# Optimization experiments

Measured on AMD Instinct MI355X. Metric: run time of the kernel, lower is better.

## Reference

```python
import jax, jax.numpy as jnp
import numpy as np

HIDDEN = 1024
N_HEAD = 16
D_HEAD = HIDDEN // N_HEAD


def setup_inputs() -> dict:
    key = jax.random.key(0)
    ks = jax.random.split(key, 12)
    B, S, H = 2, 2048, HIDDEN
    scale = 1.0 / np.sqrt(H)
    inp = {
        "q": jax.random.normal(ks[0], (B, S, H), jnp.float32),
        "k": jax.random.normal(ks[1], (B, S, H), jnp.float32),
        "v": jax.random.normal(ks[2], (B, S, H), jnp.float32),
        "mask": jnp.ones((B, 1, S, S), jnp.int32),
        "w_q": jax.random.normal(ks[3], (H, H), jnp.float32) * scale,
        "b_q": jnp.zeros((H,), jnp.float32),
        "w_k": jax.random.normal(ks[4], (H, H), jnp.float32) * scale,
        "b_k": jnp.zeros((H,), jnp.float32),
        "w_v": jax.random.normal(ks[5], (H, H), jnp.float32) * scale,
        "b_v": jnp.zeros((H,), jnp.float32),
        "w_o": jax.random.normal(ks[6], (H, H), jnp.float32) * scale,
        "b_o": jnp.zeros((H,), jnp.float32),
    }
    return inp


def reference(q, k, v, mask, w_q, b_q, w_k, b_k, w_v, b_v, w_o, b_o):
    B, Sq, H = q.shape
    Sk = k.shape[1]
    # projections (weights stored as [in, out])
    qh = (q @ w_q + b_q).reshape(B, Sq, N_HEAD, D_HEAD).transpose(0, 2, 1, 3)
    kh = (k @ w_k + b_k).reshape(B, Sk, N_HEAD, D_HEAD).transpose(0, 2, 1, 3)
    vh = (v @ w_v + b_v).reshape(B, Sk, N_HEAD, D_HEAD).transpose(0, 2, 1, 3)
    scores = jnp.einsum("bhqd,bhkd->bhqk", qh, kh) * (D_HEAD ** -0.5)
    scores = jnp.where(mask == 0, jnp.float32(-10000.0), scores)
    attn = jax.nn.softmax(scores, axis=-1)
    out = jnp.einsum("bhqk,bhkd->bhqd", attn, vh)
    out = out.transpose(0, 2, 1, 3).reshape(B, Sq, H)
    return out @ w_o + b_o
```

## Files before the change

kernel.cpp:

```cpp
#include <hip/hip_runtime.h>
#include <hip/hip_bf16.h>
#include <stdint.h>

#define S_LEN 2048
#define HID   1024
#define NHEAD 16
#define DHEAD 64
#define BATCH 2

#define QSCALE 0.18033688f
#define MASKNEG -14427.0f

typedef __bf16 bf16_t;
typedef __bf16 bf16x4 __attribute__((ext_vector_type(4)));
typedef __bf16 bf16x8 __attribute__((ext_vector_type(8)));
typedef float  f32x4  __attribute__((ext_vector_type(4)));


__device__ __forceinline__ void gl_lds16(const bf16_t* g, bf16_t* l) {
  __builtin_amdgcn_global_load_lds((const __attribute__((address_space(1))) void*)g,
                                   (__attribute__((address_space(3))) void*)l,
                                   16, 0, 0);
}

template<int TR, int TC>
__device__ __forceinline__ void stage_tile(const bf16_t* __restrict__ g, int ldg,
                                           bf16_t* lds, int wave, int lane) {
  constexpr int CH = TC / 8;
  constexpr int NINST = (TR * CH) / 64;
  #pragma unroll
  for (int i = wave; i < NINST; i += 4) {
    int slot = i * 64 + lane;
    int r  = slot / CH;
    int cs = slot & (CH - 1);
    int c  = cs ^ (r & (CH - 1));
    gl_lds16(g + (size_t)r * ldg + c * 8, lds + i * 512);
  }
}

template<int CH>
__device__ __forceinline__ bf16x8 frag_ld(const bf16_t* lds, int row, int kchunk) {
  int cs = kchunk ^ (row & (CH - 1));
  return *(const bf16x8*)(lds + (row * CH + cs) * 8);
}

__global__ __launch_bounds__(256) void cvt3(const float* __restrict__ q,
                                            const float* __restrict__ k,
                                            const float* __restrict__ v,
                                            bf16_t* __restrict__ qb,
                                            bf16_t* __restrict__ kb,
                                            bf16_t* __restrict__ vb) {
  int which = blockIdx.y;
  const float* src = which == 0 ? q : which == 1 ? k : v;
  bf16_t* dst = which == 0 ? qb : which == 1 ? kb : vb;
  size_t i = ((size_t)blockIdx.x * 256 + threadIdx.x) * 4;
  float4 u = *(const float4*)(src + i);
  bf16x4 o = {(bf16_t)u.x, (bf16_t)u.y, (bf16_t)u.z, (bf16_t)u.w};
  *(bf16x4*)(dst + i) = o;
}

__global__ __launch_bounds__(256) void transpose_w4(
    const float* __restrict__ w0, const float* __restrict__ w1,
    const float* __restrict__ w2, const float* __restrict__ w3,
    bf16_t* __restrict__ wt, int* __restrict__ flags) {
  if (blockIdx.x == 0 && blockIdx.y == 0 && blockIdx.z == 0) {
    flags[threadIdx.x] = -1;
    flags[threadIdx.x + 256] = -1;
  }
  __shared__ float t[64][65];
  const float* W = blockIdx.z == 0 ? w0 : blockIdx.z == 1 ? w1 : blockIdx.z == 2 ? w2 : w3;
  bf16_t* WT = wt + (size_t)blockIdx.z * HID * HID;
  int tx = threadIdx.x & 63, ty = threadIdx.x >> 6;
  int r0 = blockIdx.y * 64, c0 = blockIdx.x * 64;
  #pragma unroll
  for (int i = ty; i < 64; i += 4) t[i][tx] = W[(size_t)(r0 + i) * HID + c0 + tx];
  __syncthreads();
  #pragma unroll
  for (int i = ty; i < 64; i += 4) WT[(size_t)(c0 + i) * HID + r0 + tx] = (bf16_t)t[tx][i];
}

__global__ __launch_bounds__(256) void mask_flags(const int* __restrict__ mask,
                                                  int* __restrict__ flags) {
  int qtile = blockIdx.x, rg = blockIdx.y, b = blockIdx.z;
  const int* base = mask + (size_t)b * S_LEN * S_LEN
                  + (size_t)(qtile * 128 + rg * 16) * S_LEN;
  int tid = threadIdx.x;
  int kt = tid >> 4;
  int ok = 1;
  #pragma unroll
  for (int r = 0; r < 16; ++r) {
    const int4* p = (const int4*)(base + (size_t)r * S_LEN + tid * 8);
    int4 a = p[0], c = p[1];
    ok &= (a.x != 0) & (a.y != 0) & (a.z != 0) & (a.w != 0) &
          (c.x != 0) & (c.y != 0) & (c.z != 0) & (c.w != 0);
  }
  __shared__ int oks[16];
  if (tid < 16) oks[tid] = -1;
  __syncthreads();
  if (!ok) atomicAnd(&oks[kt], 0);
  __syncthreads();
  if (tid < 16 && oks[tid] == 0) atomicAnd(&flags[(b * 16 + qtile) * 16 + tid], 0);
}

__global__ __launch_bounds__(256) void qkv_gemm(
    const bf16_t* __restrict__ qb, const bf16_t* __restrict__ kb, const bf16_t* __restrict__ vb,
    const bf16_t* __restrict__ wT,
    const float* __restrict__ bq, const float* __restrict__ bk, const float* __restrict__ bv,
    bf16_t* __restrict__ Qh, bf16_t* __restrict__ Kh, bf16_t* __restrict__ VhT) {
  int mode = blockIdx.z;
  const bf16_t* A    = mode == 0 ? qb : mode == 1 ? kb : vb;
  const bf16_t* Bt   = wT + (size_t)mode * HID * HID;
  const float*  bias = mode == 0 ? bq : mode == 1 ? bk : bv;

  __shared__ __align__(16) bf16_t As[128 * 64];
  __shared__ __align__(16) bf16_t Bs[128 * 64];

  int tid = threadIdx.x, wave = tid >> 6, lane = tid & 63;
  int lane15 = lane & 15, quad = lane >> 4;
  int m0 = blockIdx.x * 128, n0 = blockIdx.y * 128;
  int wm = (wave >> 1) * 64, wn = (wave & 1) * 64;

  f32x4 zero4 = {0.f, 0.f, 0.f, 0.f};
  f32x4 acc[4][4];
  #pragma unroll
  for (int t = 0; t < 4; ++t)
    #pragma unroll
    for (int n = 0; n < 4; ++n) acc[t][n] = zero4;

  for (int k0 = 0; k0 < HID; k0 += 64) {
    stage_tile<128, 64>(A  + (size_t)m0 * HID + k0, HID, As, wave, lane);
    stage_tile<128, 64>(Bt + (size_t)n0 * HID + k0, HID, Bs, wave, lane);
    __syncthreads();
    #pragma unroll
    for (int kc = 0; kc < 2; ++kc) {
      bf16x8 af[4], bfr[4];
      #pragma unroll
      for (int t = 0; t < 4; ++t) af[t]  = frag_ld<8>(As, wm + t * 16 + lane15, kc * 4 + quad);
      #pragma unroll
      for (int n = 0; n < 4; ++n) bfr[n] = frag_ld<8>(Bs, wn + n * 16 + lane15, kc * 4 + quad);
      if (mode < 2) {
        #pragma unroll
        for (int t = 0; t < 4; ++t)
          #pragma unroll
          for (int n = 0; n < 4; ++n)
            acc[t][n] = __builtin_amdgcn_mfma_f32_16x16x32_bf16(af[t], bfr[n], acc[t][n], 0, 0, 0);
      } else {
        #pragma unroll
        for (int t = 0; t < 4; ++t)
          #pragma unroll
          for (int n = 0; n < 4; ++n)
            acc[t][n] = __builtin_amdgcn_mfma_f32_16x16x32_bf16(bfr[n], af[t], acc[t][n], 0, 0, 0);
      }
    }
    __syncthreads();
  }

  if (mode < 2) {
    float sc = (mode == 0) ? QSCALE : 1.0f;
    bf16_t* dst = (mode == 0 ? Qh : Kh);
    #pragma unroll
    for (int t = 0; t < 4; ++t) {
      #pragma unroll
      for (int n = 0; n < 4; ++n) {
        int col = n0 + wn + n * 16 + lane15;
        float bb = bias[col];
        #pragma unroll
        for (int i = 0; i < 4; ++i) {
          int row = m0 + wm + t * 16 + quad * 4 + i;
          bf16_t o = (bf16_t)((acc[t][n][i] + bb) * sc);
          int b = row >> 11, s = row & 2047;
          int h = col >> 6,  d = col & 63;
          dst[((size_t)(b * NHEAD + h) * S_LEN + s) * DHEAD + d] = o;
        }
      }
    }
  } else {
    #pragma unroll
    for (int n = 0; n < 4; ++n) {
      int dbase = n0 + wn + n * 16 + quad * 4;
      float4 bb4 = *(const float4*)(bias + dbase);
      #pragma unroll
      for (int t = 0; t < 4; ++t) {
        int token = m0 + wm + t * 16 + lane15;
        int b = token >> 11, s = token & 2047;
        #pragma unroll
        for (int i = 0; i < 4; ++i) {
          int dg = dbase + i;
          int h = dg >> 6, d = dg & 63;
          float bb = i == 0 ? bb4.x : i == 1 ? bb4.y : i == 2 ? bb4.z : bb4.w;
          VhT[((size_t)(b * NHEAD + h) * DHEAD + d) * S_LEN + s] = (bf16_t)(acc[t][n][i] + bb);
        }
      }
    }
  }
}

__global__ __launch_bounds__(256) void attn_kernel(
    const bf16_t* __restrict__ Qh, const bf16_t* __restrict__ Kh, const bf16_t* __restrict__ VhT,
    const int* __restrict__ mask, const int* __restrict__ flags,
    bf16_t* __restrict__ O) {
  __shared__ __align__(16) bf16_t Ks[2][64 * 64];
  __shared__ __align__(16) bf16_t VTs[2][80 * 64];
  __shared__ __align__(16) bf16_t Ps[128 * 64];

  int tid = threadIdx.x, wave = tid >> 6, lane = tid & 63;
  int lane15 = lane & 15, quad = lane >> 4;
  int bh = blockIdx.y, b = bh >> 4, h = bh & 15;
  int qt = blockIdx.x;
  int wrow = wave * 32;

  const bf16_t* Kbase = Kh + (size_t)bh * S_LEN * DHEAD;
  const bf16_t* Vbase = VhT + (size_t)bh * DHEAD * S_LEN;
  const int* flagrow = flags + (b * 16 + qt) * 16;

  if (tid < 64) {
    VTs[0][64 * 64 + tid] = (bf16_t)1.0f;
    VTs[1][64 * 64 + tid] = (bf16_t)1.0f;
  }

  stage_tile<128, 64>(Qh + ((size_t)bh * S_LEN + qt * 128) * DHEAD, DHEAD, Ps, wave, lane);
  stage_tile<64, 64>(Kbase, DHEAD, Ks[0], wave, lane);
  stage_tile<64, 64>(Vbase, S_LEN, VTs[0], wave, lane);
  __syncthreads();

  bf16x8 qa[2][2];
  #pragma unroll
  for (int kc = 0; kc < 2; ++kc)
    #pragma unroll
    for (int nq = 0; nq < 2; ++nq)
      qa[kc][nq] = frag_ld<8>(Ps, wrow + nq * 16 + lane15, kc * 4 + quad);

  f32x4 zero4 = {0.f, 0.f, 0.f, 0.f};
  f32x4 o_acc[2][5];
  #pragma unroll
  for (int nq = 0; nq < 2; ++nq)
    #pragma unroll
    for (int mt = 0; mt < 5; ++mt) o_acc[nq][mt] = zero4;

  int cur = 0;
  for (int kt = 0; kt < S_LEN / 64; ++kt) {
    if (kt + 1 < S_LEN / 64) {
      stage_tile<64, 64>(Kbase + (size_t)(kt + 1) * 64 * DHEAD, DHEAD, Ks[cur ^ 1], wave, lane);
      stage_tile<64, 64>(Vbase + (kt + 1) * 64, S_LEN, VTs[cur ^ 1], wave, lane);
    }
    const bf16_t* Kc = Ks[cur];
    const bf16_t* Vc = VTs[cur];

    f32x4 sa[2][4];
    {
      bf16x8 kf[4];
      #pragma unroll
      for (int mc = 0; mc < 4; ++mc) kf[mc] = frag_ld<8>(Kc, mc * 16 + lane15, quad);
      __builtin_amdgcn_s_setprio(1);
      #pragma unroll
      for (int nq = 0; nq < 2; ++nq)
        #pragma unroll
        for (int mc = 0; mc < 4; ++mc)
          sa[nq][mc] = __builtin_amdgcn_mfma_f32_16x16x32_bf16(kf[mc], qa[0][nq], zero4, 0, 0, 0);
      __builtin_amdgcn_s_setprio(0);
      #pragma unroll
      for (int mc = 0; mc < 4; ++mc) kf[mc] = frag_ld<8>(Kc, mc * 16 + lane15, 4 + quad);
      __builtin_amdgcn_s_setprio(1);
      #pragma unroll
      for (int nq = 0; nq < 2; ++nq)
        #pragma unroll
        for (int mc = 0; mc < 4; ++mc)
          sa[nq][mc] = __builtin_amdgcn_mfma_f32_16x16x32_bf16(kf[mc], qa[1][nq], sa[nq][mc], 0, 0, 0);
      __builtin_amdgcn_s_setprio(0);
    }

    if (flagrow[kt >> 1] == 0) {
      #pragma unroll
      for (int nq = 0; nq < 2; ++nq)
        #pragma unroll
        for (int mc = 0; mc < 4; ++mc)
          #pragma unroll
          for (int i = 0; i < 4; ++i) {
            int q = qt * 128 + wrow + nq * 16 + lane15;
            int c = kt * 64 + mc * 16 + quad * 4 + i;
            if (mask[(size_t)b * S_LEN * S_LEN + (size_t)q * S_LEN + c] == 0)
              sa[nq][mc][i] = MASKNEG;
          }
    }

    #pragma unroll
    for (int nq = 0; nq < 2; ++nq) {
      int q = wrow + nq * 16 + lane15;
      #pragma unroll
      for (int mc = 0; mc < 4; ++mc) {
        bf16x4 pk = {(bf16_t)exp2f(sa[nq][mc][0]), (bf16_t)exp2f(sa[nq][mc][1]),
                     (bf16_t)exp2f(sa[nq][mc][2]), (bf16_t)exp2f(sa[nq][mc][3])};
        int chunk = mc * 2 + (quad >> 1);
        int slot = chunk ^ (q & 7);
        *(bf16x4*)(Ps + q * 64 + slot * 8 + (quad & 1) * 4) = pk;
      }
    }

    #pragma unroll
    for (int kc = 0; kc < 2; ++kc) {
      bf16x8 vf[5], pf[2];
      #pragma unroll
      for (int mt = 0; mt < 5; ++mt) vf[mt] = frag_ld<8>(Vc, mt * 16 + lane15, kc * 4 + quad);
      #pragma unroll
      for (int nq = 0; nq < 2; ++nq) pf[nq] = frag_ld<8>(Ps, wrow + nq * 16 + lane15, kc * 4 + quad);
      __builtin_amdgcn_s_setprio(1);
      #pragma unroll
      for (int nq = 0; nq < 2; ++nq)
        #pragma unroll
        for (int mt = 0; mt < 5; ++mt)
          o_acc[nq][mt] = __builtin_amdgcn_mfma_f32_16x16x32_bf16(vf[mt], pf[nq], o_acc[nq][mt], 0, 0, 0);
      __builtin_amdgcn_s_setprio(0);
    }

    __syncthreads();
    cur ^= 1;
  }

  #pragma unroll
  for (int nq = 0; nq < 2; ++nq) {
    float lval = __shfl(o_acc[nq][4][0], lane15);
    float inv = 1.0f / lval;
    int s = qt * 128 + wrow + nq * 16 + lane15;
    size_t orow = ((size_t)b * S_LEN + s) * HID + h * DHEAD;
    #pragma unroll
    for (int mt = 0; mt < 4; ++mt) {
      bf16x4 ov = {(bf16_t)(o_acc[nq][mt][0] * inv), (bf16_t)(o_acc[nq][mt][1] * inv),
                   (bf16_t)(o_acc[nq][mt][2] * inv), (bf16_t)(o_acc[nq][mt][3] * inv)};
      *(bf16x4*)(O + orow + mt * 16 + quad * 4) = ov;
    }
  }
}

__global__ __launch_bounds__(256) void oproj_gemm(
    const bf16_t* __restrict__ A, const bf16_t* __restrict__ Bt,
    const float* __restrict__ bias, float* __restrict__ out) {
  __shared__ __align__(16) bf16_t As[128 * 64];
  __shared__ __align__(16) bf16_t Bs[128 * 64];

  int tid = threadIdx.x, wave = tid >> 6, lane = tid & 63;
  int lane15 = lane & 15, quad = lane >> 4;
  int m0 = blockIdx.x * 128, n0 = blockIdx.y * 128;
  int wm = (wave >> 1) * 64, wn = (wave & 1) * 64;

  f32x4 zero4 = {0.f, 0.f, 0.f, 0.f};
  f32x4 acc[4][4];
  #pragma unroll
  for (int t = 0; t < 4; ++t)
    #pragma unroll
    for (int n = 0; n < 4; ++n) acc[t][n] = zero4;

  for (int k0 = 0; k0 < HID; k0 += 64) {
    stage_tile<128, 64>(A  + (size_t)m0 * HID + k0, HID, As, wave, lane);
    stage_tile<128, 64>(Bt + (size_t)n0 * HID + k0, HID, Bs, wave, lane);
    __syncthreads();
    #pragma unroll
    for (int kc = 0; kc < 2; ++kc) {
      bf16x8 af[4], bfr[4];
      #pragma unroll
      for (int t = 0; t < 4; ++t) af[t]  = frag_ld<8>(As, wm + t * 16 + lane15, kc * 4 + quad);
      #pragma unroll
      for (int n = 0; n < 4; ++n) bfr[n] = frag_ld<8>(Bs, wn + n * 16 + lane15, kc * 4 + quad);
      #pragma unroll
      for (int t = 0; t < 4; ++t)
        #pragma unroll
        for (int n = 0; n < 4; ++n)
          acc[t][n] = __builtin_amdgcn_mfma_f32_16x16x32_bf16(af[t], bfr[n], acc[t][n], 0, 0, 0);
    }
    __syncthreads();
  }

  #pragma unroll
  for (int t = 0; t < 4; ++t) {
    #pragma unroll
    for (int n = 0; n < 4; ++n) {
      int col = n0 + wn + n * 16 + lane15;
      float bb = bias[col];
      #pragma unroll
      for (int i = 0; i < 4; ++i) {
        int row = m0 + wm + t * 16 + quad * 4 + i;
        out[(size_t)row * HID + col] = acc[t][n][i] + bb;
      }
    }
  }
}

extern "C" void kernel_launch(void* const* d_in, const int* in_sizes, int n_in,
                              void* d_out, int out_size, void* d_ws, size_t ws_size,
                              hipStream_t stream) {
  (void)in_sizes; (void)n_in; (void)out_size; (void)ws_size;
  const float* q  = (const float*)d_in[0];
  const float* k  = (const float*)d_in[1];
  const float* v  = (const float*)d_in[2];
  const int*  mask = (const int*)d_in[3];
  const float* wq = (const float*)d_in[4];
  const float* bq = (const float*)d_in[5];
  const float* wk = (const float*)d_in[6];
  const float* bk = (const float*)d_in[7];
  const float* wv = (const float*)d_in[8];
  const float* bv = (const float*)d_in[9];
  const float* wo = (const float*)d_in[10];
  const float* bo = (const float*)d_in[11];

  char* ws = (char*)d_ws;
  bf16_t* wT    = (bf16_t*)(ws);
  bf16_t* Qh    = (bf16_t*)(ws + (8u  << 20));
  bf16_t* Kh    = (bf16_t*)(ws + (16u << 20));
  bf16_t* VhT   = (bf16_t*)(ws + (24u << 20));
  bf16_t* qb    = (bf16_t*)(ws + (32u << 20));
  bf16_t* kb    = (bf16_t*)(ws + (40u << 20));
  bf16_t* vb    = (bf16_t*)(ws + (48u << 20));
  int* flags    = (int*)(ws + (56u << 20));
  bf16_t* Obuf  = qb;

  cvt3<<<dim3(4096, 3), 256, 0, stream>>>(q, k, v, qb, kb, vb);
  transpose_w4<<<dim3(16, 16, 4), 256, 0, stream>>>(wq, wk, wv, wo, wT, flags);
  mask_flags<<<dim3(16, 8, 2), 256, 0, stream>>>(mask, flags);
  qkv_gemm<<<dim3(32, 8, 3), 256, 0, stream>>>(qb, kb, vb, wT, bq, bk, bv, Qh, Kh, VhT);
  attn_kernel<<<dim3(16, 32), 256, 0, stream>>>(Qh, Kh, VhT, mask, flags, Obuf);
  oproj_gemm<<<dim3(32, 8), 256, 0, stream>>>(Obuf, wT + (size_t)3 * HID * HID, bo, (float*)d_out);
}
```

Measured before the change: 279.3 us.

## Use eight waves per attention block with sixteen query rows each

```diff
diff --git a/kernel.cpp b/kernel.cpp
--- a/kernel.cpp
+++ b/kernel.cpp
@@ -23,13 +23,13 @@
                                    16, 0, 0);
 }
 
-template<int TR, int TC>
+template<int TR, int TC, int NW = 4>
 __device__ __forceinline__ void stage_tile(const bf16_t* __restrict__ g, int ldg,
                                            bf16_t* lds, int wave, int lane) {
   constexpr int CH = TC / 8;
   constexpr int NINST = (TR * CH) / 64;
   #pragma unroll
-  for (int i = wave; i < NINST; i += 4) {
+  for (int i = wave; i < NINST; i += NW) {
     int slot = i * 64 + lane;
     int r  = slot / CH;
     int cs = slot & (CH - 1);
@@ -195,7 +195,7 @@
   }
 }
 
-__global__ __launch_bounds__(256) void attn_kernel(
+__global__ __launch_bounds__(512) void attn_kernel(
     const bf16_t* __restrict__ Qh, const bf16_t* __restrict__ Kh, const bf16_t* __restrict__ VhT,
     const int* __restrict__ mask, const int* __restrict__ flags,
     bf16_t* __restrict__ O) {
@@ -207,7 +207,7 @@
   int lane15 = lane & 15, quad = lane >> 4;
   int bh = blockIdx.y, b = bh >> 4, h = bh & 15;
   int qt = blockIdx.x;
-  int wrow = wave * 32;
+  int wrow = wave * 16;
 
   const bf16_t* Kbase = Kh + (size_t)bh * S_LEN * DHEAD;
   const bf16_t* Vbase = VhT + (size_t)bh * DHEAD * S_LEN;
@@ -218,78 +218,67 @@
     VTs[1][64 * 64 + tid] = (bf16_t)1.0f;
   }
 
-  stage_tile<128, 64>(Qh + ((size_t)bh * S_LEN + qt * 128) * DHEAD, DHEAD, Ps, wave, lane);
-  stage_tile<64, 64>(Kbase, DHEAD, Ks[0], wave, lane);
-  stage_tile<64, 64>(Vbase, S_LEN, VTs[0], wave, lane);
+  stage_tile<128, 64, 8>(Qh + ((size_t)bh * S_LEN + qt * 128) * DHEAD, DHEAD, Ps, wave, lane);
+  stage_tile<64, 64, 8>(Kbase, DHEAD, Ks[0], wave, lane);
+  stage_tile<64, 64, 8>(Vbase, S_LEN, VTs[0], wave, lane);
   __syncthreads();
 
-  bf16x8 qa[2][2];
+  bf16x8 qa[2];
   #pragma unroll
   for (int kc = 0; kc < 2; ++kc)
-    #pragma unroll
-    for (int nq = 0; nq < 2; ++nq)
-      qa[kc][nq] = frag_ld<8>(Ps, wrow + nq * 16 + lane15, kc * 4 + quad);
+    qa[kc] = frag_ld<8>(Ps, wrow + lane15, kc * 4 + quad);
 
   f32x4 zero4 = {0.f, 0.f, 0.f, 0.f};
-  f32x4 o_acc[2][5];
-  #pragma unroll
-  for (int nq = 0; nq < 2; ++nq)
-    #pragma unroll
-    for (int mt = 0; mt < 5; ++mt) o_acc[nq][mt] = zero4;
+  f32x4 o_acc[5];
+  #pragma unroll
+  for (int mt = 0; mt < 5; ++mt) o_acc[mt] = zero4;
 
   int cur = 0;
   for (int kt = 0; kt < S_LEN / 64; ++kt) {
     if (kt + 1 < S_LEN / 64) {
-      stage_tile<64, 64>(Kbase + (size_t)(kt + 1) * 64 * DHEAD, DHEAD, Ks[cur ^ 1], wave, lane);
-      stage_tile<64, 64>(Vbase + (kt + 1) * 64, S_LEN, VTs[cur ^ 1], wave, lane);
+      stage_tile<64, 64, 8>(Kbase + (size_t)(kt + 1) * 64 * DHEAD, DHEAD, Ks[cur ^ 1], wave, lane);
+      stage_tile<64, 64, 8>(Vbase + (kt + 1) * 64, S_LEN, VTs[cur ^ 1], wave, lane);
     }
     const bf16_t* Kc = Ks[cur];
     const bf16_t* Vc = VTs[cur];
 
-    f32x4 sa[2][4];
+    f32x4 sa[4];
     {
       bf16x8 kf[4];
       #pragma unroll
       for (int mc = 0; mc < 4; ++mc) kf[mc] = frag_ld<8>(Kc, mc * 16 + lane15, quad);
       __builtin_amdgcn_s_setprio(1);
       #pragma unroll
-      for (int nq = 0; nq < 2; ++nq)
-        #pragma unroll
-        for (int mc = 0; mc < 4; ++mc)
-          sa[nq][mc] = __builtin_amdgcn_mfma_f32_16x16x32_bf16(kf[mc], qa[0][nq], zero4, 0, 0, 0);
+      for (int mc = 0; mc < 4; ++mc)
+        sa[mc] = __builtin_amdgcn_mfma_f32_16x16x32_bf16(kf[mc], qa[0], zero4, 0, 0, 0);
       __builtin_amdgcn_s_setprio(0);
       #pragma unroll
       for (int mc = 0; mc < 4; ++mc) kf[mc] = frag_ld<8>(Kc, mc * 16 + lane15, 4 + quad);
       __builtin_amdgcn_s_setprio(1);
       #pragma unroll
-      for (int nq = 0; nq < 2; ++nq)
-        #pragma unroll
-        for (int mc = 0; mc < 4; ++mc)
-          sa[nq][mc] = __builtin_amdgcn_mfma_f32_16x16x32_bf16(kf[mc], qa[1][nq], sa[nq][mc], 0, 0, 0);
+      for (int mc = 0; mc < 4; ++mc)
+        sa[mc] = __builtin_amdgcn_mfma_f32_16x16x32_bf16(kf[mc], qa[1], sa[mc], 0, 0, 0);
       __builtin_amdgcn_s_setprio(0);
     }
 
     if (flagrow[kt >> 1] == 0) {
-      #pragma unroll
-      for (int nq = 0; nq < 2; ++nq)
-        #pragma unroll
-        for (int mc = 0; mc < 4; ++mc)
-          #pragma unroll
-          for (int i = 0; i < 4; ++i) {
-            int q = qt * 128 + wrow + nq * 16 + lane15;
-            int c = kt * 64 + mc * 16 + quad * 4 + i;
-            if (mask[(size_t)b * S_LEN * S_LEN + (size_t)q * S_LEN + c] == 0)
-              sa[nq][mc][i] = MASKNEG;
-          }
-    }
-
-    #pragma unroll
-    for (int nq = 0; nq < 2; ++nq) {
-      int q = wrow + nq * 16 + lane15;
+      int q = qt * 128 + wrow + lane15;
+      #pragma unroll
+      for (int mc = 0; mc < 4; ++mc)
+        #pragma unroll
+        for (int i = 0; i < 4; ++i) {
+          int c = kt * 64 + mc * 16 + quad * 4 + i;
+          if (mask[(size_t)b * S_LEN * S_LEN + (size_t)q * S_LEN + c] == 0)
+            sa[mc][i] = MASKNEG;
+        }
+    }
+
+    {
+      int q = wrow + lane15;
       #pragma unroll
       for (int mc = 0; mc < 4; ++mc) {
-        bf16x4 pk = {(bf16_t)exp2f(sa[nq][mc][0]), (bf16_t)exp2f(sa[nq][mc][1]),
-                     (bf16_t)exp2f(sa[nq][mc][2]), (bf16_t)exp2f(sa[nq][mc][3])};
+        bf16x4 pk = {(bf16_t)exp2f(sa[mc][0]), (bf16_t)exp2f(sa[mc][1]),
+                     (bf16_t)exp2f(sa[mc][2]), (bf16_t)exp2f(sa[mc][3])};
         int chunk = mc * 2 + (quad >> 1);
         int slot = chunk ^ (q & 7);
         *(bf16x4*)(Ps + q * 64 + slot * 8 + (quad & 1) * 4) = pk;
@@ -298,17 +287,14 @@
 
     #pragma unroll
     for (int kc = 0; kc < 2; ++kc) {
-      bf16x8 vf[5], pf[2];
+      bf16x8 vf[5], pf;
       #pragma unroll
       for (int mt = 0; mt < 5; ++mt) vf[mt] = frag_ld<8>(Vc, mt * 16 + lane15, kc * 4 + quad);
-      #pragma unroll
-      for (int nq = 0; nq < 2; ++nq) pf[nq] = frag_ld<8>(Ps, wrow + nq * 16 + lane15, kc * 4 + quad);
+      pf = frag_ld<8>(Ps, wrow + lane15, kc * 4 + quad);
       __builtin_amdgcn_s_setprio(1);
       #pragma unroll
-      for (int nq = 0; nq < 2; ++nq)
-        #pragma unroll
-        for (int mt = 0; mt < 5; ++mt)
-          o_acc[nq][mt] = __builtin_amdgcn_mfma_f32_16x16x32_bf16(vf[mt], pf[nq], o_acc[nq][mt], 0, 0, 0);
+      for (int mt = 0; mt < 5; ++mt)
+        o_acc[mt] = __builtin_amdgcn_mfma_f32_16x16x32_bf16(vf[mt], pf, o_acc[mt], 0, 0, 0);
       __builtin_amdgcn_s_setprio(0);
     }
 
@@ -316,16 +302,15 @@
     cur ^= 1;
   }
 
-  #pragma unroll
-  for (int nq = 0; nq < 2; ++nq) {
-    float lval = __shfl(o_acc[nq][4][0], lane15);
+  {
+    float lval = __shfl(o_acc[4][0], lane15);
     float inv = 1.0f / lval;
-    int s = qt * 128 + wrow + nq * 16 + lane15;
+    int s = qt * 128 + wrow + lane15;
     size_t orow = ((size_t)b * S_LEN + s) * HID + h * DHEAD;
     #pragma unroll
     for (int mt = 0; mt < 4; ++mt) {
-      bf16x4 ov = {(bf16_t)(o_acc[nq][mt][0] * inv), (bf16_t)(o_acc[nq][mt][1] * inv),
-                   (bf16_t)(o_acc[nq][mt][2] * inv), (bf16_t)(o_acc[nq][mt][3] * inv)};
+      bf16x4 ov = {(bf16_t)(o_acc[mt][0] * inv), (bf16_t)(o_acc[mt][1] * inv),
+                   (bf16_t)(o_acc[mt][2] * inv), (bf16_t)(o_acc[mt][3] * inv)};
       *(bf16x4*)(O + orow + mt * 16 + quad * 4) = ov;
     }
   }
@@ -416,6 +401,6 @@
   transpose_w4<<<dim3(16, 16, 4), 256, 0, stream>>>(wq, wk, wv, wo, wT, flags);
   mask_flags<<<dim3(16, 8, 2), 256, 0, stream>>>(mask, flags);
   qkv_gemm<<<dim3(32, 8, 3), 256, 0, stream>>>(qb, kb, vb, wT, bq, bk, bv, Qh, Kh, VhT);
-  attn_kernel<<<dim3(16, 32), 256, 0, stream>>>(Qh, Kh, VhT, mask, flags, Obuf);
+  attn_kernel<<<dim3(16, 32), 512, 0, stream>>>(Qh, Kh, VhT, mask, flags, Obuf);
   oproj_gemm<<<dim3(32, 8), 256, 0, stream>>>(Obuf, wT + (size_t)3 * HID * HID, bo, (float*)d_out);
 }
```

Result: faster. 272.4 us (-2.5%).
